# Kernel tuning notes

Measured on AMD Instinct MI355X. Metric: run time of the kernel, lower is better.

Reference implementation:

```python
import jax, jax.numpy as jnp
import numpy as np

D_MODEL = 768
N_LAYERS = 2
D_STATE = 16
D_CONV = 4
EXPAND = 2
D_INNER = EXPAND * D_MODEL
DT_RANK = (D_MODEL + 15) // 16  # ceil(d_model/16) = 48
BATCH, SEQ = 2, 2048


def setup_inputs() -> dict:
    key = jax.random.key(0)
    ks = jax.random.split(key, 12)
    s = 0.02
    x = jax.random.normal(ks[0], (BATCH, SEQ, D_MODEL), jnp.float32)
    in_proj_w = jax.random.normal(ks[1], (N_LAYERS, 2 * D_INNER, D_MODEL), jnp.float32) * s
    conv_w = jax.random.normal(ks[2], (N_LAYERS, D_INNER, D_CONV), jnp.float32) * s
    conv_b = jnp.zeros((N_LAYERS, D_INNER), jnp.float32)
    x_proj_w = jax.random.normal(ks[3], (N_LAYERS, DT_RANK + 2 * D_STATE, D_INNER), jnp.float32) * s
    dt_proj_w = jax.random.normal(ks[4], (N_LAYERS, D_INNER, DT_RANK), jnp.float32) * (DT_RANK ** -0.5)
    # mamba dt bias init: softplus^{-1} of dt ~ Uniform[1e-3, 0.1] in log space
    rng = np.random.default_rng(0)
    dt = np.exp(rng.uniform(np.log(1e-3), np.log(0.1), size=(N_LAYERS, D_INNER)))
    dt_proj_b = jnp.asarray(dt + np.log(-np.expm1(-dt)), jnp.float32)
    A_log = jnp.log(jnp.broadcast_to(jnp.arange(1, D_STATE + 1, dtype=jnp.float32), (N_LAYERS, D_INNER, D_STATE)))
    D_param = jnp.ones((N_LAYERS, D_INNER), jnp.float32)
    out_proj_w = jax.random.normal(ks[5], (N_LAYERS, D_MODEL, D_INNER), jnp.float32) * s
    ln_w = jnp.ones((N_LAYERS, D_MODEL), jnp.float32)
    ln_b = jnp.zeros((N_LAYERS, D_MODEL), jnp.float32)
    fnorm_w = jnp.ones((D_MODEL,), jnp.float32)
    fnorm_b = jnp.zeros((D_MODEL,), jnp.float32)
    proj_w = jax.random.normal(ks[6], (D_MODEL, D_MODEL), jnp.float32) * s
    proj_b = jnp.zeros((D_MODEL,), jnp.float32)
    return {"x": x, "in_proj_w": in_proj_w, "conv_w": conv_w, "conv_b": conv_b,
            "x_proj_w": x_proj_w, "dt_proj_w": dt_proj_w, "dt_proj_b": dt_proj_b,
            "A_log": A_log, "D_param": D_param, "out_proj_w": out_proj_w,
            "ln_w": ln_w, "ln_b": ln_b, "fnorm_w": fnorm_w, "fnorm_b": fnorm_b,
            "proj_w": proj_w, "proj_b": proj_b}


def _layer_norm(x, w, b, eps=1e-5):
    mu = jnp.mean(x, axis=-1, keepdims=True)
    var = jnp.mean(jnp.square(x - mu), axis=-1, keepdims=True)
    return (x - mu) * jax.lax.rsqrt(var + eps) * w + b


def _selective_scan(u, dt, A, Bm, Cm, Dp):
    # u, dt: [B,L,di]; A: [di,ds]; Bm, Cm: [B,L,ds]; Dp: [di]
    def step(h, inp):
        dt_t, B_t, C_t, u_t = inp  # [B,di],[B,ds],[B,ds],[B,di]
        dA = jnp.exp(dt_t[..., None] * A)              # [B,di,ds]
        h = dA * h + (dt_t * u_t)[..., None] * B_t[:, None, :]
        y = jnp.einsum('bds,bs->bd', h, C_t)
        return h, y
    bsz = u.shape[0]
    h0 = jnp.zeros((bsz, A.shape[0], A.shape[1]), u.dtype)
    xs = (jnp.swapaxes(dt, 0, 1), jnp.swapaxes(Bm, 0, 1), jnp.swapaxes(Cm, 0, 1), jnp.swapaxes(u, 0, 1))
    _, ys = jax.lax.scan(step, h0, xs)                 # ys: [L,B,di]
    return jnp.swapaxes(ys, 0, 1) + u * Dp


def _mamba_block(x, p):
    xz = jnp.einsum('bld,ed->ble', x, p['in_proj_w'])  # [B,L,2*di]
    u, z = xz[..., :D_INNER], xz[..., D_INNER:]
    # depthwise causal conv1d
    u_c = jnp.swapaxes(u, 1, 2)                        # [B,di,L]
    kern = p['conv_w'][:, None, :]                     # [di,1,dc]
    u_c = jax.lax.conv_general_dilated(u_c, kern, (1,), [(D_CONV - 1, 0)],
                                       feature_group_count=D_INNER,
                                       dimension_numbers=('NCH', 'OIH', 'NCH'))
    u = jax.nn.silu(jnp.swapaxes(u_c + p['conv_b'][:, None], 1, 2))
    x_dbl = jnp.einsum('bld,ed->ble', u, p['x_proj_w'])
    dt = jax.nn.softplus(jnp.einsum('blr,dr->bld', x_dbl[..., :DT_RANK], p['dt_proj_w']) + p['dt_proj_b'])
    Bm = x_dbl[..., DT_RANK:DT_RANK + D_STATE]
    Cm = x_dbl[..., DT_RANK + D_STATE:]
    A = -jnp.exp(p['A_log'])
    y = _selective_scan(u, dt, A, Bm, Cm, p['D_param'])
    y = y * jax.nn.silu(z)
    return jnp.einsum('ble,de->bld', y, p['out_proj_w'])


def reference(x, in_proj_w, conv_w, conv_b, x_proj_w, dt_proj_w, dt_proj_b,
              A_log, D_param, out_proj_w, ln_w, ln_b, fnorm_w, fnorm_b, proj_w, proj_b):
    h = x
    for i in range(N_LAYERS):
        p = {'in_proj_w': in_proj_w[i], 'conv_w': conv_w[i], 'conv_b': conv_b[i],
             'x_proj_w': x_proj_w[i], 'dt_proj_w': dt_proj_w[i], 'dt_proj_b': dt_proj_b[i],
             'A_log': A_log[i], 'D_param': D_param[i], 'out_proj_w': out_proj_w[i]}
        h = h + _mamba_block(_layer_norm(h, ln_w[i], ln_b[i]), p)  # dropout=0 (eval)
    h = _layer_norm(h, fnorm_w, fnorm_b)
    return jnp.einsum('bld,ed->ble', h, proj_w) + proj_b
```

## Files before the change

kernel.cpp:

```cpp
#include <hip/hip_runtime.h>
#include <math.h>

#define D_MODEL   768
#define N_LAYERS  2
#define D_STATE   16
#define D_CONV    4
#define D_INNER   1536
#define DT_RANK   48
#define BATCH     2
#define SEQ       2048
#define NTOK      (BATCH * SEQ)
#define XZ_DIM    (2 * D_INNER)
#define XDBL_DIM  (DT_RANK + 2 * D_STATE)

#define CHUNKS    64
#define TCHUNK    (SEQ / CHUNKS)
#define NCH       (BATCH * CHUNKS * D_INNER)
#define SCAN_ELT  (NCH * D_STATE)

typedef short short8   __attribute__((ext_vector_type(8)));
typedef float floatx4  __attribute__((ext_vector_type(4)));
typedef unsigned short ushort8 __attribute__((ext_vector_type(8)));

__device__ __forceinline__ unsigned short f2bf(float f) {
    unsigned int u = __float_as_uint(f);
    u += 0x7FFFu + ((u >> 16) & 1u);
    return (unsigned short)(u >> 16);
}
__device__ __forceinline__ float bf2f(unsigned short h) {
    return __uint_as_float((unsigned int)h << 16);
}
__device__ __forceinline__ float softplusf(float x) {
    return (x > 20.f) ? x : log1pf(expf(x));
}

__device__ __forceinline__ void gload16(const unsigned short* g, unsigned short* l) {
    __builtin_amdgcn_global_load_lds(
        (const __attribute__((address_space(1))) unsigned int*)g,
        (__attribute__((address_space(3))) unsigned int*)l, 16, 0, 0);
}

#define CW_IN   (N_LAYERS * XZ_DIM * D_MODEL / 8)
#define CW_OUT  (N_LAYERS * D_MODEL * D_INNER / 8)
#define CW_PROJ (D_MODEL * D_MODEL / 8)
#define CW_X    (N_LAYERS * 128 * D_INNER / 8)
#define CW_DT   (N_LAYERS * D_INNER * 64 / 8)
#define CW_TOT  (CW_IN + CW_OUT + CW_PROJ + CW_X + CW_DT)

__device__ __forceinline__ void cvt8(const float* __restrict__ s,
                                     unsigned short* __restrict__ d) {
    const float4 a = ((const float4*)s)[0];
    const float4 b = ((const float4*)s)[1];
    ushort8 o;
    o[0] = f2bf(a.x); o[1] = f2bf(a.y); o[2] = f2bf(a.z); o[3] = f2bf(a.w);
    o[4] = f2bf(b.x); o[5] = f2bf(b.y); o[6] = f2bf(b.z); o[7] = f2bf(b.w);
    *(ushort8*)d = o;
}

__global__ __launch_bounds__(256) void convert_all_k(
    const float* __restrict__ in_w,  const float* __restrict__ out_w,
    const float* __restrict__ proj_w,const float* __restrict__ x_w,
    const float* __restrict__ dt_w,
    unsigned short* __restrict__ w_in,  unsigned short* __restrict__ w_out,
    unsigned short* __restrict__ w_proj,unsigned short* __restrict__ w_x,
    unsigned short* __restrict__ w_dt)
{
    int g = blockIdx.x * 256 + threadIdx.x;
    if (g >= CW_TOT) return;
    if (g < CW_IN)  { cvt8(in_w  + (size_t)g * 8, w_in  + (size_t)g * 8); return; }
    g -= CW_IN;
    if (g < CW_OUT) { cvt8(out_w + (size_t)g * 8, w_out + (size_t)g * 8); return; }
    g -= CW_OUT;
    if (g < CW_PROJ){ cvt8(proj_w+ (size_t)g * 8, w_proj+ (size_t)g * 8); return; }
    g -= CW_PROJ;
    if (g < CW_X) {
        const long e0 = (long)g * 8;
        const int k0 = e0 % 1536;
        const int n  = (e0 / 1536) % 128;
        const int L  = e0 / (1536 * 128);
        if (n < XDBL_DIM)
            cvt8(x_w + ((size_t)(L * XDBL_DIM + n) * 1536 + k0), w_x + e0);
        else
            *(ushort8*)(w_x + e0) = (ushort8)0;
        return;
    }
    g -= CW_X;
    {
        const long e0 = (long)g * 8;
        const int k0 = e0 % 64;
        const int n  = (e0 / 64) % 1536;
        const int L  = e0 / (64 * 1536);
        if (k0 < DT_RANK)
            cvt8(dt_w + ((size_t)(L * 1536 + n) * DT_RANK + k0), w_dt + e0);
        else
            *(ushort8*)(w_dt + e0) = (ushort8)0;
    }
}

__global__ __launch_bounds__(256) void convert_flat8_k(
    const float* __restrict__ src, unsigned short* __restrict__ dst, int n8)
{
    const int i = blockIdx.x * 256 + threadIdx.x;
    if (i >= n8) return;
    cvt8(src + (size_t)i * 8, dst + (size_t)i * 8);
}

__global__ __launch_bounds__(256) void layernorm_k(
    const float* __restrict__ x, const float* __restrict__ w,
    const float* __restrict__ b, unsigned short* __restrict__ out)
{
    const int tok = blockIdx.x;
    const int tid = threadIdx.x;
    const float* xr = x + (long)tok * D_MODEL;
    float v[3];
    float s = 0.f, sq = 0.f;
#pragma unroll
    for (int j = 0; j < 3; j++) {
        v[j] = xr[tid + j * 256];
        s += v[j];
        sq += v[j] * v[j];
    }
#pragma unroll
    for (int off = 32; off > 0; off >>= 1) {
        s  += __shfl_xor(s, off, 64);
        sq += __shfl_xor(sq, off, 64);
    }
    __shared__ float ssum[4], ssq[4];
    if ((tid & 63) == 0) { ssum[tid >> 6] = s; ssq[tid >> 6] = sq; }
    __syncthreads();
    const float S  = ssum[0] + ssum[1] + ssum[2] + ssum[3];
    const float SQ = ssq[0] + ssq[1] + ssq[2] + ssq[3];
    const float mean = S * (1.f / D_MODEL);
    const float var  = SQ * (1.f / D_MODEL) - mean * mean;
    const float rstd = rsqrtf(var + 1e-5f);
    unsigned short* orow = out + (long)tok * D_MODEL;
#pragma unroll
    for (int j = 0; j < 3; j++) {
        const int c = tid + j * 256;
        orow[c] = f2bf((v[j] - mean) * rstd * w[c] + b[c]);
    }
}

__global__ __launch_bounds__(256) void gemm128_k(
    const unsigned short* __restrict__ A, int lda,
    const unsigned short* __restrict__ B, int ldb,
    unsigned short* __restrict__ Cb, int ldc, int K)
{
    __shared__ unsigned short sm[128 * 128];
    unsigned short* As = sm;
    unsigned short* Bs = sm + 8192;
    const int tid = threadIdx.x;
    const int m0 = blockIdx.y * 128;
    const int n0 = blockIdx.x * 128;

    const unsigned short* agp[4];
    const unsigned short* bgp[4];
    unsigned short* alp[4];
    unsigned short* blp[4];
#pragma unroll
    for (int q = 0; q < 4; q++) {
        const int flat = q * 256 + tid;
        const int row  = flat >> 3;
        const int c    = flat & 7;
        const int g    = (c - row) & 7;
        agp[q] = A + (size_t)(m0 + row) * lda + g * 8;
        bgp[q] = B + (size_t)(n0 + row) * ldb + g * 8;
        alp[q] = As + flat * 8;
        blp[q] = Bs + flat * 8;
    }

    const int lane = tid & 63;
    const int w    = tid >> 6;
    const int wm   = (w >> 1) * 64;
    const int wn   = (w & 1) * 64;
    const int fr   = lane & 15;
    const int fq   = lane >> 4;

    floatx4 acc[4][4];
#pragma unroll
    for (int i = 0; i < 4; i++)
#pragma unroll
        for (int j = 0; j < 4; j++)
            acc[i][j] = (floatx4)0.f;

    for (int k0 = 0; k0 < K; k0 += 64) {
#pragma unroll
        for (int q = 0; q < 4; q++) {
            gload16(agp[q], alp[q]); gload16(bgp[q], blp[q]);
            agp[q] += 64; bgp[q] += 64;
        }
        __syncthreads();
#pragma unroll
        for (int kk = 0; kk < 2; kk++) {
            short8 av[4], bv[4];
#pragma unroll
            for (int i = 0; i < 4; i++) {
                const int r = wm + i * 16 + fr;
                av[i] = *(const short8*)&As[r * 64 + (((kk * 4 + fq) + r) & 7) * 8];
            }
#pragma unroll
            for (int j = 0; j < 4; j++) {
                const int r = wn + j * 16 + fr;
                bv[j] = *(const short8*)&Bs[r * 64 + (((kk * 4 + fq) + r) & 7) * 8];
            }
#pragma unroll
            for (int i = 0; i < 4; i++)
#pragma unroll
                for (int j = 0; j < 4; j++)
                    acc[i][j] = __builtin_amdgcn_mfma_f32_16x16x32_bf16(
                        av[i], bv[j], acc[i][j], 0, 0, 0);
        }
        __syncthreads();
    }

#pragma unroll
    for (int i = 0; i < 4; i++)
#pragma unroll
        for (int j = 0; j < 4; j++)
#pragma unroll
            for (int r = 0; r < 4; r++)
                sm[(wm + i * 16 + fq * 4 + r) * 128 + (wn + j * 16 + fr)] =
                    f2bf(acc[i][j][r]);
    __syncthreads();
#pragma unroll
    for (int s = 0; s < 8; s++) {
        const int f   = s * 256 + tid;
        const int row = f >> 4;
        const int c16 = f & 15;
        *(ushort8*)(Cb + (size_t)(m0 + row) * ldc + n0 + c16 * 8) =
            *(const ushort8*)&sm[row * 128 + c16 * 8];
    }
}

template <int ATOMIC, int BIAS, int SP, int WF32, int WBF16>
__global__ __launch_bounds__(256) void gemm64_k(
    const unsigned short* __restrict__ A, int lda,
    const unsigned short* __restrict__ B, int ldb,
    const float* __restrict__ bias,
    float* __restrict__ Cf, unsigned short* __restrict__ Cb, int ldc,
    int N, int klen)
{
    __shared__ unsigned short sm[64 * 64];
    unsigned short* As = sm;
    unsigned short* Bs = sm + 2048;
    const int tid = threadIdx.x;
    const int m0 = blockIdx.y * 64;
    const int n0 = blockIdx.x * 64;
    const int kb = blockIdx.z * klen;

    const int srow = tid >> 2;
    const int sc   = tid & 3;
    const int sg_  = (sc - (srow >> 1)) & 3;
    const unsigned short* ag = A + (size_t)(m0 + srow) * lda + kb + sg_ * 8;
    const unsigned short* bg = B + (size_t)(n0 + srow) * ldb + kb + sg_ * 8;
    unsigned short* la = As + tid * 8;
    unsigned short* lb = Bs + tid * 8;

    const int lane = tid & 63;
    const int w    = tid >> 6;
    const int wm   = w * 16;
    const int fr   = lane & 15;
    const int fq   = lane >> 4;

    floatx4 acc[4];
#pragma unroll
    for (int j = 0; j < 4; j++) acc[j] = (floatx4)0.f;

    for (int k0 = 0; k0 < klen; k0 += 32) {
        gload16(ag, la); gload16(bg, lb);
        ag += 32; bg += 32;
        __syncthreads();
        const int ar = wm + fr;
        const short8 av = *(const short8*)&As[ar * 32 + (((fq + (ar >> 1)) & 3) * 8)];
        short8 bv[4];
#pragma unroll
        for (int j = 0; j < 4; j++) {
            const int br = j * 16 + fr;
            bv[j] = *(const short8*)&Bs[br * 32 + (((fq + (br >> 1)) & 3) * 8)];
        }
#pragma unroll
        for (int j = 0; j < 4; j++)
            acc[j] = __builtin_amdgcn_mfma_f32_16x16x32_bf16(av, bv[j], acc[j], 0, 0, 0);
        __syncthreads();
    }

    if (WBF16) {
#pragma unroll
        for (int j = 0; j < 4; j++) {
            const int col = j * 16 + fr;
            float bvv = 0.f;
            if (BIAS) bvv = bias[n0 + col];
#pragma unroll
            for (int r = 0; r < 4; r++) {
                float v = acc[j][r];
                if (BIAS) v += bvv;
                if (SP)   v = softplusf(v);
                sm[(wm + fq * 4 + r) * 64 + col] = f2bf(v);
            }
        }
        __syncthreads();
#pragma unroll
        for (int s = 0; s < 2; s++) {
            const int f   = s * 256 + tid;
            const int row = f >> 3;
            const int c8  = f & 7;
            *(ushort8*)(Cb + (size_t)(m0 + row) * ldc + n0 + c8 * 8) =
                *(const ushort8*)&sm[row * 64 + c8 * 8];
        }
    } else {
#pragma unroll
        for (int j = 0; j < 4; j++) {
            const int col = n0 + j * 16 + fr;
            if (col >= N) continue;
            float bvv = 0.f;
            if (BIAS) bvv = bias[col];
#pragma unroll
            for (int r = 0; r < 4; r++) {
                const int row = m0 + wm + fq * 4 + r;
                const size_t idx = (size_t)row * ldc + col;
                float v = acc[j][r];
                if (BIAS) v += bvv;
                if (SP)   v = softplusf(v);
                if (ATOMIC) atomicAdd(&Cf[idx], v);
                else if (WF32) Cf[idx] = v;
            }
        }
    }
}

__global__ __launch_bounds__(256) void conv_silu_k(
    const unsigned short* __restrict__ xz, const float* __restrict__ w,
    const float* __restrict__ bconv, unsigned short* __restrict__ ub,
    float* __restrict__ xdbl_zero)
{
    const int i = blockIdx.x * 256 + threadIdx.x;
    if (i >= NTOK * (D_INNER / 8)) return;
    if (i < NTOK * XDBL_DIM) xdbl_zero[i] = 0.f;
    const int dg  = i % (D_INNER / 8);
    const int tok = i / (D_INNER / 8);
    const int t   = tok % SEQ;
    const long rowbase = (long)tok * XZ_DIM;

    float acc[8];
    float4 wv[8];
#pragma unroll
    for (int e = 0; e < 8; e++) {
        const int d = dg + 192 * e;
        acc[e] = bconv[d];
        wv[e]  = ((const float4*)w)[d];
    }
#pragma unroll
    for (int k = 0; k < D_CONV; k++) {
        const int off = k - (D_CONV - 1);
        if (t + off < 0) continue;
        const long base = rowbase + (long)off * XZ_DIM;
#pragma unroll
        for (int e = 0; e < 8; e++) {
            const int d = dg + 192 * e;
            const float xv = bf2f(xz[base + d]);
            const float wk = (k == 0) ? wv[e].x : (k == 1) ? wv[e].y
                           : (k == 2) ? wv[e].z : wv[e].w;
            acc[e] = fmaf(wk, xv, acc[e]);
        }
    }
    unsigned short* urow = ub + (long)tok * D_INNER;
#pragma unroll
    for (int e = 0; e < 8; e++) {
        const int d = dg + 192 * e;
        const float sig = 1.f / (1.f + __expf(-acc[e]));
        urow[d] = f2bf(acc[e] * sig);
    }
}

__global__ __launch_bounds__(256) void scan_phase1(
    const unsigned short* __restrict__ dtbuf, const unsigned short* __restrict__ ubuf,
    const float* __restrict__ xdbl,  const float* __restrict__ A_log,
    float* __restrict__ dtsum, float4* __restrict__ S4)
{
    const int ch = blockIdx.x * 256 + threadIdx.x;
    const int d  = ch % D_INNER;
    const int bc = ch / D_INNER;
    const int c  = bc % CHUNKS;
    const int b  = bc / CHUNKS;

    float As[16];
    {
        const float4* ap = (const float4*)(A_log + d * D_STATE);
#pragma unroll
        for (int j = 0; j < 4; j++) {
            const float4 a = ap[j];
            As[4*j+0] = -__expf(a.x); As[4*j+1] = -__expf(a.y);
            As[4*j+2] = -__expf(a.z); As[4*j+3] = -__expf(a.w);
        }
    }
    const long tok0 = (long)b * SEQ + c * TCHUNK;
    const unsigned short* dtp = dtbuf + tok0 * D_INNER + d;
    const unsigned short* up  = ubuf  + tok0 * D_INNER + d;
    const float* xp  = xdbl  + tok0 * XDBL_DIM;

    float S[16];
#pragma unroll
    for (int s = 0; s < 16; s++) S[s] = 0.f;
    float dts = 0.f;

    for (int l = 0; l < TCHUNK; l++) {
        const float dt = bf2f(dtp[(long)l * D_INNER]);
        const float u  = bf2f(up [(long)l * D_INNER]);
        const float4* B4p = (const float4*)(xp + (long)l * XDBL_DIM + DT_RANK);
        float B[16];
#pragma unroll
        for (int j = 0; j < 4; j++) {
            const float4 bb = B4p[j];
            B[4*j+0] = bb.x; B[4*j+1] = bb.y; B[4*j+2] = bb.z; B[4*j+3] = bb.w;
        }
        const float du = dt * u;
        dts += dt;
#pragma unroll
        for (int s = 0; s < 16; s++) {
            const float e = __expf(dt * As[s]);
            S[s] = fmaf(e, S[s], du * B[s]);
        }
    }
    dtsum[ch] = dts;
#pragma unroll
    for (int j = 0; j < 4; j++) {
        float4 sv;
        sv.x = S[4*j+0]; sv.y = S[4*j+1]; sv.z = S[4*j+2]; sv.w = S[4*j+3];
        S4[(size_t)j * NCH + ch] = sv;
    }
}

__global__ __launch_bounds__(64) void scan_phase2(
    const float* __restrict__ dtsum, const float* __restrict__ A_log,
    float4* __restrict__ H4, const float4* __restrict__ S4)
{
    const int t = blockIdx.x * 64 + threadIdx.x;
    const int sg = t & 3;
    const int rest = t >> 2;
    const int d = rest % D_INNER;
    const int b = rest / D_INNER;
    const float4 a = *(const float4*)(A_log + d * D_STATE + sg * 4);
    const float A0 = -__expf(a.x), A1 = -__expf(a.y);
    const float A2 = -__expf(a.z), A3 = -__expf(a.w);
    float4* Hp = H4 + (size_t)sg * NCH;
    const float4* Sp = S4 + (size_t)sg * NCH;
    float4 H = make_float4(0.f, 0.f, 0.f, 0.f);
    for (int c = 0; c < CHUNKS; c++) {
        const size_t ci = (size_t)(b * CHUNKS + c) * D_INNER + d;
        const float ds = dtsum[ci];
        const float4 Sv = Sp[ci];
        Hp[ci] = H;
        H.x = fmaf(__expf(A0 * ds), H.x, Sv.x);
        H.y = fmaf(__expf(A1 * ds), H.y, Sv.y);
        H.z = fmaf(__expf(A2 * ds), H.z, Sv.z);
        H.w = fmaf(__expf(A3 * ds), H.w, Sv.w);
    }
}

__global__ __launch_bounds__(256) void scan_phase3(
    const unsigned short* __restrict__ dtbuf, const unsigned short* __restrict__ ubuf,
    const unsigned short* __restrict__ xz,    const float* __restrict__ xdbl,
    const float* __restrict__ A_log, const float* __restrict__ Dp,
    const float4* __restrict__ H4,   unsigned short* __restrict__ ybuf)
{
    const int ch = blockIdx.x * 256 + threadIdx.x;
    const int d  = ch % D_INNER;
    const int bc = ch / D_INNER;
    const int c  = bc % CHUNKS;
    const int b  = bc / CHUNKS;

    float As[16];
    {
        const float4* ap = (const float4*)(A_log + d * D_STATE);
#pragma unroll
        for (int j = 0; j < 4; j++) {
            const float4 a = ap[j];
            As[4*j+0] = -__expf(a.x); As[4*j+1] = -__expf(a.y);
            As[4*j+2] = -__expf(a.z); As[4*j+3] = -__expf(a.w);
        }
    }
    float h[16];
#pragma unroll
    for (int j = 0; j < 4; j++) {
        const float4 hv = H4[(size_t)j * NCH + ch];
        h[4*j+0] = hv.x; h[4*j+1] = hv.y; h[4*j+2] = hv.z; h[4*j+3] = hv.w;
    }
    const float Dv = Dp[d];
    const long tok0 = (long)b * SEQ + c * TCHUNK;
    const unsigned short* dtp = dtbuf + tok0 * D_INNER + d;
    const unsigned short* up  = ubuf  + tok0 * D_INNER + d;
    const unsigned short* zp  = xz    + tok0 * XZ_DIM + D_INNER + d;
    const float* xp  = xdbl  + tok0 * XDBL_DIM;
    unsigned short* yp = ybuf + tok0 * D_INNER + d;

    for (int l = 0; l < TCHUNK; l++) {
        const float dt = bf2f(dtp[(long)l * D_INNER]);
        const float u  = bf2f(up [(long)l * D_INNER]);
        const float z  = bf2f(zp [(long)l * XZ_DIM]);
        const float4* B4p = (const float4*)(xp + (long)l * XDBL_DIM + DT_RANK);
        float B[16], C[16];
#pragma unroll
        for (int j = 0; j < 4; j++) {
            const float4 bb = B4p[j];
            B[4*j+0] = bb.x; B[4*j+1] = bb.y; B[4*j+2] = bb.z; B[4*j+3] = bb.w;
        }
#pragma unroll
        for (int j = 0; j < 4; j++) {
            const float4 cc = B4p[4 + j];
            C[4*j+0] = cc.x; C[4*j+1] = cc.y; C[4*j+2] = cc.z; C[4*j+3] = cc.w;
        }
        const float du = dt * u;
        float y = 0.f;
#pragma unroll
        for (int s = 0; s < 16; s++) {
            const float e = __expf(dt * As[s]);
            h[s] = fmaf(e, h[s], du * B[s]);
            y = fmaf(h[s], C[s], y);
        }
        y = fmaf(u, Dv, y);
        const float sig = 1.f / (1.f + __expf(-z));
        yp[(long)l * D_INNER] = f2bf(y * (z * sig));
    }
}

extern "C" void kernel_launch(void* const* d_in, const int* in_sizes, int n_in,
                              void* d_out, int out_size, void* d_ws, size_t ws_size,
                              hipStream_t stream)
{
    const float* x         = (const float*)d_in[0];
    const float* in_proj_w = (const float*)d_in[1];
    const float* conv_w    = (const float*)d_in[2];
    const float* conv_b    = (const float*)d_in[3];
    const float* x_proj_w  = (const float*)d_in[4];
    const float* dt_proj_w = (const float*)d_in[5];
    const float* dt_proj_b = (const float*)d_in[6];
    const float* A_log     = (const float*)d_in[7];
    const float* D_param   = (const float*)d_in[8];
    const float* out_proj_w= (const float*)d_in[9];
    const float* ln_w      = (const float*)d_in[10];
    const float* ln_b      = (const float*)d_in[11];
    const float* fnorm_w   = (const float*)d_in[12];
    const float* fnorm_b   = (const float*)d_in[13];
    const float* proj_w    = (const float*)d_in[14];
    const float* proj_b    = (const float*)d_in[15];

    float* ws    = (float*)d_ws;
    float* h     = ws;
    float* xdbl  = h    + (long)NTOK * D_MODEL;
    float* Hbuf  = xdbl + (long)NTOK * XDBL_DIM;
    float* dtsum = Hbuf + SCAN_ELT;
    float* fend  = dtsum + NCH;

    unsigned short* us      = (unsigned short*)fend;
    unsigned short* hln_bf  = us;
    unsigned short* xz_bf   = hln_bf + (long)NTOK * D_MODEL;
    unsigned short* u_bf    = xz_bf  + (long)NTOK * XZ_DIM;
    unsigned short* xdbl_bf = u_bf   + (long)NTOK * D_INNER;
    unsigned short* dt_bf   = xdbl_bf+ (long)NTOK * XDBL_DIM;
    unsigned short* y_bf    = dt_bf  + (long)NTOK * D_INNER;
    unsigned short* w_in    = y_bf   + (long)NTOK * D_INNER;
    unsigned short* w_out   = w_in   + (long)N_LAYERS * XZ_DIM * D_MODEL;
    unsigned short* w_proj  = w_out  + (long)N_LAYERS * D_MODEL * D_INNER;
    unsigned short* w_x     = w_proj + (long)D_MODEL * D_MODEL;
    unsigned short* w_dt    = w_x    + (long)N_LAYERS * 128 * D_INNER;

    float4* S4 = (float4*)d_out;
    float4* H4 = (float4*)Hbuf;

    convert_all_k<<<(CW_TOT + 255) / 256, 256, 0, stream>>>(
        in_proj_w, out_proj_w, proj_w, x_proj_w, dt_proj_w,
        w_in, w_out, w_proj, w_x, w_dt);

    hipMemcpyAsync(h, x, (long)NTOK * D_MODEL * sizeof(float),
                   hipMemcpyDeviceToDevice, stream);

    for (int layer = 0; layer < N_LAYERS; layer++) {
        layernorm_k<<<NTOK, 256, 0, stream>>>(
            h, ln_w + layer * D_MODEL, ln_b + layer * D_MODEL, hln_bf);

        gemm128_k<<<dim3(XZ_DIM / 128, NTOK / 128), 256, 0, stream>>>(
            hln_bf, D_MODEL, w_in + (long)layer * XZ_DIM * D_MODEL, D_MODEL,
            xz_bf, XZ_DIM, D_MODEL);

        conv_silu_k<<<(NTOK * D_INNER / 8 + 255) / 256, 256, 0, stream>>>(
            xz_bf, conv_w + (long)layer * D_INNER * D_CONV,
            conv_b + (long)layer * D_INNER, u_bf, xdbl);

        gemm64_k<1, 0, 0, 0, 0><<<dim3(2, NTOK / 64, 8), 256, 0, stream>>>(
            u_bf, D_INNER, w_x + (long)layer * 128 * D_INNER, D_INNER,
            nullptr, xdbl, nullptr, XDBL_DIM, XDBL_DIM, D_INNER / 8);
        convert_flat8_k<<<(NTOK * XDBL_DIM / 8 + 255) / 256, 256, 0, stream>>>(
            xdbl, xdbl_bf, NTOK * XDBL_DIM / 8);

        gemm64_k<0, 1, 1, 0, 1><<<dim3(D_INNER / 64, NTOK / 64), 256, 0, stream>>>(
            xdbl_bf, XDBL_DIM, w_dt + (long)layer * D_INNER * 64, 64,
            dt_proj_b + layer * D_INNER, nullptr, dt_bf, D_INNER, D_INNER, 64);

        scan_phase1<<<NCH / 256, 256, 0, stream>>>(
            dt_bf, u_bf, xdbl, A_log + (long)layer * D_INNER * D_STATE, dtsum, S4);
        scan_phase2<<<(BATCH * D_INNER * 4) / 64, 64, 0, stream>>>(
            dtsum, A_log + (long)layer * D_INNER * D_STATE, H4, S4);
        scan_phase3<<<NCH / 256, 256, 0, stream>>>(
            dt_bf, u_bf, xz_bf, xdbl,
            A_log + (long)layer * D_INNER * D_STATE,
            D_param + (long)layer * D_INNER, H4, y_bf);

        gemm64_k<1, 0, 0, 0, 0><<<dim3(D_MODEL / 64, NTOK / 64, 2), 256, 0, stream>>>(
            y_bf, D_INNER, w_out + (long)layer * D_MODEL * D_INNER, D_INNER,
            nullptr, h, nullptr, D_MODEL, D_MODEL, D_INNER / 2);
    }

    layernorm_k<<<NTOK, 256, 0, stream>>>(h, fnorm_w, fnorm_b, hln_bf);

    gemm64_k<0, 1, 0, 1, 0><<<dim3(D_MODEL / 64, NTOK / 64), 256, 0, stream>>>(
        hln_bf, D_MODEL, w_proj, D_MODEL, proj_b,
        (float*)d_out, nullptr, D_MODEL, D_MODEL, D_MODEL);
}
```

Baseline: 540.6 us.

## Replace atomic split-K accumulation with partial planes reduced in consumer kernels

Split-K GEMMs for x_proj and out_proj now write per-split partial results to separate fp32 planes instead of using atomicAdd into zeroed buffers. A dedicated reduce kernel sums the x_proj partials and emits both fp32 and bf16 copies, replacing the separate convert kernel and the zeroing in conv. The out_proj partials are folded into the following layernorm, which adds the residual and writes h back. This removes atomic contention and zero-initialisation, at the cost of extra workspace and more memory traffic to read the partial planes.

```diff
diff --git a/kernel.cpp b/kernel.cpp
--- a/kernel.cpp
+++ b/kernel.cpp
@@ -17,6 +17,9 @@
 #define TCHUNK    (SEQ / CHUNKS)
 #define NCH       (BATCH * CHUNKS * D_INNER)
 #define SCAN_ELT  (NCH * D_STATE)
+
+#define XSPLIT    8
+#define OSPLIT    2
 
 typedef short short8   __attribute__((ext_vector_type(8)));
 typedef float floatx4  __attribute__((ext_vector_type(4)));
@@ -97,28 +100,52 @@
     }
 }
 
-__global__ __launch_bounds__(256) void convert_flat8_k(
-    const float* __restrict__ src, unsigned short* __restrict__ dst, int n8)
+__global__ __launch_bounds__(256) void reduce_x_k(
+    const float* __restrict__ pX, float* __restrict__ xdbl,
+    unsigned short* __restrict__ xdbl_bf)
 {
     const int i = blockIdx.x * 256 + threadIdx.x;
-    if (i >= n8) return;
-    cvt8(src + (size_t)i * 8, dst + (size_t)i * 8);
-}
-
+    if (i >= NTOK * XDBL_DIM / 8) return;
+    float4 s0 = make_float4(0.f, 0.f, 0.f, 0.f);
+    float4 s1 = make_float4(0.f, 0.f, 0.f, 0.f);
+#pragma unroll
+    for (int p = 0; p < XSPLIT; p++) {
+        const float4* pp = (const float4*)(pX + (size_t)p * NTOK * XDBL_DIM) + 2 * i;
+        const float4 a = pp[0], b = pp[1];
+        s0.x += a.x; s0.y += a.y; s0.z += a.z; s0.w += a.w;
+        s1.x += b.x; s1.y += b.y; s1.z += b.z; s1.w += b.w;
+    }
+    ((float4*)xdbl)[2 * i]     = s0;
+    ((float4*)xdbl)[2 * i + 1] = s1;
+    ushort8 o;
+    o[0] = f2bf(s0.x); o[1] = f2bf(s0.y); o[2] = f2bf(s0.z); o[3] = f2bf(s0.w);
+    o[4] = f2bf(s1.x); o[5] = f2bf(s1.y); o[6] = f2bf(s1.z); o[7] = f2bf(s1.w);
+    ((ushort8*)xdbl_bf)[i] = o;
+}
+
+template <int ADDP>
 __global__ __launch_bounds__(256) void layernorm_k(
-    const float* __restrict__ x, const float* __restrict__ w,
-    const float* __restrict__ b, unsigned short* __restrict__ out)
+    float* __restrict__ x, const float* __restrict__ P,
+    const float* __restrict__ w, const float* __restrict__ b,
+    unsigned short* __restrict__ out)
 {
     const int tok = blockIdx.x;
     const int tid = threadIdx.x;
-    const float* xr = x + (long)tok * D_MODEL;
+    float* xr = x + (long)tok * D_MODEL;
     float v[3];
     float s = 0.f, sq = 0.f;
 #pragma unroll
     for (int j = 0; j < 3; j++) {
-        v[j] = xr[tid + j * 256];
-        s += v[j];
-        sq += v[j] * v[j];
+        const int c = tid + j * 256;
+        float vv = xr[c];
+        if (ADDP) {
+            const size_t idx = (size_t)tok * D_MODEL + c;
+            vv += P[idx] + P[(size_t)NTOK * D_MODEL + idx];
+            xr[c] = vv;
+        }
+        v[j] = vv;
+        s += vv;
+        sq += vv * vv;
     }
 #pragma unroll
     for (int off = 32; off > 0; off >>= 1) {
@@ -232,13 +259,13 @@
     }
 }
 
-template <int ATOMIC, int BIAS, int SP, int WF32, int WBF16>
+template <int BIAS, int SP, int WF32, int WBF16>
 __global__ __launch_bounds__(256) void gemm64_k(
     const unsigned short* __restrict__ A, int lda,
     const unsigned short* __restrict__ B, int ldb,
     const float* __restrict__ bias,
     float* __restrict__ Cf, unsigned short* __restrict__ Cb, int ldc,
-    int N, int klen)
+    int N, int klen, size_t planeStride)
 {
     __shared__ unsigned short sm[64 * 64];
     unsigned short* As = sm;
@@ -247,6 +274,7 @@
     const int m0 = blockIdx.y * 64;
     const int n0 = blockIdx.x * 64;
     const int kb = blockIdx.z * klen;
+    float* Cfp = Cf + (size_t)blockIdx.z * planeStride;
 
     const int srow = tid >> 2;
     const int sc   = tid & 3;
@@ -307,7 +335,7 @@
             *(ushort8*)(Cb + (size_t)(m0 + row) * ldc + n0 + c8 * 8) =
                 *(const ushort8*)&sm[row * 64 + c8 * 8];
         }
-    } else {
+    } else if (WF32) {
 #pragma unroll
         for (int j = 0; j < 4; j++) {
             const int col = n0 + j * 16 + fr;
@@ -317,12 +345,10 @@
 #pragma unroll
             for (int r = 0; r < 4; r++) {
                 const int row = m0 + wm + fq * 4 + r;
-                const size_t idx = (size_t)row * ldc + col;
                 float v = acc[j][r];
                 if (BIAS) v += bvv;
                 if (SP)   v = softplusf(v);
-                if (ATOMIC) atomicAdd(&Cf[idx], v);
-                else if (WF32) Cf[idx] = v;
+                Cfp[(size_t)row * ldc + col] = v;
             }
         }
     }
@@ -330,12 +356,10 @@
 
 __global__ __launch_bounds__(256) void conv_silu_k(
     const unsigned short* __restrict__ xz, const float* __restrict__ w,
-    const float* __restrict__ bconv, unsigned short* __restrict__ ub,
-    float* __restrict__ xdbl_zero)
+    const float* __restrict__ bconv, unsigned short* __restrict__ ub)
 {
     const int i = blockIdx.x * 256 + threadIdx.x;
     if (i >= NTOK * (D_INNER / 8)) return;
-    if (i < NTOK * XDBL_DIM) xdbl_zero[i] = 0.f;
     const int dg  = i % (D_INNER / 8);
     const int tok = i / (D_INNER / 8);
     const int t   = tok % SEQ;
@@ -549,7 +573,9 @@
     float* xdbl  = h    + (long)NTOK * D_MODEL;
     float* Hbuf  = xdbl + (long)NTOK * XDBL_DIM;
     float* dtsum = Hbuf + SCAN_ELT;
-    float* fend  = dtsum + NCH;
+    float* pX    = dtsum + NCH;
+    float* pOut  = pX + (long)XSPLIT * NTOK * XDBL_DIM;
+    float* fend  = pOut + (long)OSPLIT * NTOK * D_MODEL;
 
     unsigned short* us      = (unsigned short*)fend;
     unsigned short* hln_bf  = us;
@@ -575,8 +601,12 @@
                    hipMemcpyDeviceToDevice, stream);
 
     for (int layer = 0; layer < N_LAYERS; layer++) {
-        layernorm_k<<<NTOK, 256, 0, stream>>>(
-            h, ln_w + layer * D_MODEL, ln_b + layer * D_MODEL, hln_bf);
+        if (layer == 0)
+            layernorm_k<0><<<NTOK, 256, 0, stream>>>(
+                h, nullptr, ln_w + layer * D_MODEL, ln_b + layer * D_MODEL, hln_bf);
+        else
+            layernorm_k<1><<<NTOK, 256, 0, stream>>>(
+                h, pOut, ln_w + layer * D_MODEL, ln_b + layer * D_MODEL, hln_bf);
 
         gemm128_k<<<dim3(XZ_DIM / 128, NTOK / 128), 256, 0, stream>>>(
             hln_bf, D_MODEL, w_in + (long)layer * XZ_DIM * D_MODEL, D_MODEL,
@@ -584,17 +614,18 @@
 
         conv_silu_k<<<(NTOK * D_INNER / 8 + 255) / 256, 256, 0, stream>>>(
             xz_bf, conv_w + (long)layer * D_INNER * D_CONV,
-            conv_b + (long)layer * D_INNER, u_bf, xdbl);
-
-        gemm64_k<1, 0, 0, 0, 0><<<dim3(2, NTOK / 64, 8), 256, 0, stream>>>(
+            conv_b + (long)layer * D_INNER, u_bf);
+
+        gemm64_k<0, 0, 1, 0><<<dim3(2, NTOK / 64, XSPLIT), 256, 0, stream>>>(
             u_bf, D_INNER, w_x + (long)layer * 128 * D_INNER, D_INNER,
-            nullptr, xdbl, nullptr, XDBL_DIM, XDBL_DIM, D_INNER / 8);
-        convert_flat8_k<<<(NTOK * XDBL_DIM / 8 + 255) / 256, 256, 0, stream>>>(
-            xdbl, xdbl_bf, NTOK * XDBL_DIM / 8);
-
-        gemm64_k<0, 1, 1, 0, 1><<<dim3(D_INNER / 64, NTOK / 64), 256, 0, stream>>>(
+            nullptr, pX, nullptr, XDBL_DIM, XDBL_DIM, D_INNER / XSPLIT,
+            (size_t)NTOK * XDBL_DIM);
+        reduce_x_k<<<(NTOK * XDBL_DIM / 8 + 255) / 256, 256, 0, stream>>>(
+            pX, xdbl, xdbl_bf);
+
+        gemm64_k<1, 1, 0, 1><<<dim3(D_INNER / 64, NTOK / 64), 256, 0, stream>>>(
             xdbl_bf, XDBL_DIM, w_dt + (long)layer * D_INNER * 64, 64,
-            dt_proj_b + layer * D_INNER, nullptr, dt_bf, D_INNER, D_INNER, 64);
+            dt_proj_b + layer * D_INNER, nullptr, dt_bf, D_INNER, D_INNER, 64, 0);
 
         scan_phase1<<<NCH / 256, 256, 0, stream>>>(
             dt_bf, u_bf, xdbl, A_log + (long)layer * D_INNER * D_STATE, dtsum, S4);
@@ -605,14 +636,15 @@
             A_log + (long)layer * D_INNER * D_STATE,
             D_param + (long)layer * D_INNER, H4, y_bf);
 
-        gemm64_k<1, 0, 0, 0, 0><<<dim3(D_MODEL / 64, NTOK / 64, 2), 256, 0, stream>>>(
+        gemm64_k<0, 0, 1, 0><<<dim3(D_MODEL / 64, NTOK / 64, OSPLIT), 256, 0, stream>>>(
             y_bf, D_INNER, w_out + (long)layer * D_MODEL * D_INNER, D_INNER,
-            nullptr, h, nullptr, D_MODEL, D_MODEL, D_INNER / 2);
-    }
-
-    layernorm_k<<<NTOK, 256, 0, stream>>>(h, fnorm_w, fnorm_b, hln_bf);
-
-    gemm64_k<0, 1, 0, 1, 0><<<dim3(D_MODEL / 64, NTOK / 64), 256, 0, stream>>>(
+            nullptr, pOut, nullptr, D_MODEL, D_MODEL, D_INNER / OSPLIT,
+            (size_t)NTOK * D_MODEL);
+    }
+
+    layernorm_k<1><<<NTOK, 256, 0, stream>>>(h, pOut, fnorm_w, fnorm_b, hln_bf);
+
+    gemm64_k<1, 0, 1, 0><<<dim3(D_MODEL / 64, NTOK / 64), 256, 0, stream>>>(
         hln_bf, D_MODEL, w_proj, D_MODEL, proj_b,
-        (float*)d_out, nullptr, D_MODEL, D_MODEL, D_MODEL);
-}
+        (float*)d_out, nullptr, D_MODEL, D_MODEL, D_MODEL, 0);
+}
```

After: 516.5 us. 1.05x faster.
